# Kernel optimization log

Measured on AMD Instinct MI355X. Metric: run time of the kernel, lower is better.

Reference implementation:

```python
import jax, jax.numpy as jnp
import numpy as np

B, S, E, H = 4096, 200, 64, 128
V_U0, V_U1, V_I = 100000, 1000, 1000000

def setup_inputs() -> dict:
    key = jax.random.key(0)
    ks = jax.random.split(key, 16)
    s = 0.05
    return {
        'user_features': jax.random.randint(ks[0], (B, 2), 0, V_U1, dtype=jnp.int32),
        'target_item_features': jax.random.randint(ks[1], (B, 1), 0, V_I, dtype=jnp.int32),
        'behavior_sequence': jax.random.randint(ks[2], (B, S, 1), 0, V_I, dtype=jnp.int32),
        'emb_user0': jax.random.normal(ks[3], (V_U0, E), jnp.float32) * s,
        'emb_user1': jax.random.normal(ks[4], (V_U1, E), jnp.float32) * s,
        'emb_item': jax.random.normal(ks[5], (V_I, E), jnp.float32) * s,
        'att_w1': jax.random.normal(ks[6], (4 * E, H), jnp.float32) * s,
        'att_b1': jnp.zeros((H,), jnp.float32),
        'att_w2': jax.random.normal(ks[7], (H, 1), jnp.float32) * s,
        'att_b2': jnp.zeros((1,), jnp.float32),
        'fc_w1': jax.random.normal(ks[8], (4 * E, H), jnp.float32) * s,
        'fc_b1': jnp.zeros((H,), jnp.float32),
        'fc_w2': jax.random.normal(ks[9], (H, 1), jnp.float32) * s,
        'fc_b2': jnp.zeros((1,), jnp.float32),
    }

def reference(user_features, target_item_features, behavior_sequence,
              emb_user0, emb_user1, emb_item,
              att_w1, att_b1, att_w2, att_b2,
              fc_w1, fc_b1, fc_w2, fc_b2):
    # embedding gathers
    user_embeds = jnp.concatenate([emb_user0[user_features[:, 0]],
                                   emb_user1[user_features[:, 1]]], axis=-1)  # [B, 2E]
    target = emb_item[target_item_features[:, 0]]                              # [B, E]
    behavior = emb_item[behavior_sequence[:, :, 0]]                            # [B, S, E]
    t = target[:, None, :]                                                     # [B, 1, E]
    t_exp = jnp.broadcast_to(t, behavior.shape)
    att_in = jnp.concatenate([behavior, t_exp, behavior - t, behavior * t], axis=-1)  # [B, S, 4E]
    # attention MLP -> scores
    h = jax.nn.relu(jnp.einsum('bsd,dh->bsh', att_in, att_w1) + att_b1)
    scores = (jnp.einsum('bsh,ho->bso', h, att_w2) + att_b2)[..., 0]           # [B, S]
    weights = jax.nn.softmax(scores, axis=1)
    user_interest = jnp.einsum('bse,bs->be', behavior, weights)                # [B, E]
    combined = jnp.concatenate([user_embeds, user_interest, target], axis=-1)  # [B, 4E]
    out = jax.nn.relu(combined @ fc_w1 + fc_b1) @ fc_w2 + fc_b2                # [B, 1]
    return out
```

## Files before the change

kernel.cpp:

```cpp
#include <hip/hip_runtime.h>
#include <math.h>


#define S_LEN 200
#define S_PAD 208

typedef __attribute__((ext_vector_type(8))) short short8;
typedef __attribute__((ext_vector_type(4))) float f32x4;

__device__ __forceinline__ unsigned short f2b(float f) {
  union { float f; unsigned u; } x; x.f = f;
  unsigned r = x.u + 0x7fffu + ((x.u >> 16) & 1u);
  return (unsigned short)(r >> 16);
}
__device__ __forceinline__ float b2f(unsigned short h) {
  union { unsigned u; float f; } x; x.u = ((unsigned)h) << 16; return x.f;
}
__device__ __forceinline__ unsigned cvt_pk_bf16(float lo, float hi) {
  unsigned r;
  asm("v_cvt_pk_bf16_f32 %0, %1, %2" : "=v"(r) : "v"(lo), "v"(hi));
  return r;
}

__device__ __forceinline__ int swzB(int row, int col) {
  int byte = row * 128 + col * 2;
  byte ^= (row & 7) << 4;
  return byte >> 1;
}
__device__ __forceinline__ int swzW(int row, int col) {
  int byte = row * 512 + col * 2;
  byte ^= (row & 7) << 4;
  return byte >> 1;
}

__device__ __forceinline__ void async_g2l_16(const void* g, void* l) {
  __builtin_amdgcn_global_load_lds(
      (const __attribute__((address_space(1))) void*)g,
      (__attribute__((address_space(3))) void*)l, 16, 0, 0);
}

template <int CTRL>
__device__ __forceinline__ float dpp_add(float v) {
  const int t = __builtin_amdgcn_mov_dpp(__float_as_int(v), CTRL, 0xF, 0xF, true);
  return v + __int_as_float(t);
}
__device__ __forceinline__ float rowReduce16(float v) {
  v = dpp_add<0xB1>(v);
  v = dpp_add<0x4E>(v);
  v = dpp_add<0x124>(v);
  v = dpp_add<0x128>(v);
  return v;
}
__device__ __forceinline__ float permAdd16(float p) {
  float a = p, b = p;
  asm("v_permlane16_swap_b32 %0, %1" : "+v"(a), "+v"(b));
  return a + b;
}
__device__ __forceinline__ float permAdd32(float p) {
  float a = p, b = p;
  asm("v_permlane32_swap_b32 %0, %1" : "+v"(a), "+v"(b));
  return a + b;
}
__device__ __forceinline__ float waveSum64(float v) {
  return permAdd32(permAdd16(rowReduce16(v)));
}

#define WS_COMB 0
#define WS_AT   2097152
#define WS_DT   2113536
#define WS_BM   2129920
#define WS_FW1T 2146304
#define WS_CH   2211840
#define WS_TS   4308992

__global__ __launch_bounds__(256)
void din_prep(const float* __restrict__ aw1, const float* __restrict__ fw1,
              char* __restrict__ ws)
{
  unsigned short* ATc  = (unsigned short*)(ws + WS_AT);
  unsigned short* DTc  = (unsigned short*)(ws + WS_DT);
  unsigned short* Bm   = (unsigned short*)(ws + WS_BM);
  unsigned short* FW1T = (unsigned short*)(ws + WS_FW1T);
  const int blk = blockIdx.x, tid = threadIdx.x;

  if (blk < 32) {
    const int i = blk * 256 + tid;
    const int h = i >> 6, d = i & 63;
    const float a  = aw1[d * 128 + h];
    const float c  = aw1[(128 + d) * 128 + h];
    const float dd = aw1[(192 + d) * 128 + h];
    const int hg = h >> 5, ht = (h >> 4) & 1, hl = h & 15;
    const int kk = d >> 5, rq = (d >> 3) & 3, j = d & 7;
    const int o = (hg * 2 + ht) * 1024 + kk * 512 + rq * 128 + hl * 8 + j;
    ATc[o] = f2b(a + c);
    DTc[o] = f2b(dd);
  } else if (blk < 64) {
    const int jj = (blk - 32) * 256 + tid;
    const int d = jj >> 7, h = jj & 127;
    Bm[jj] = f2b(aw1[(64 + d) * 128 + h] - aw1[(128 + d) * 128 + h]);
  } else {
    const int i = (blk - 64) * 256 + tid;
    const int o = 2 * i;
    const int h = o >> 9;
    const int rr = o & 511;
    const int d = (rr ^ ((h & 7) << 4)) >> 1;
    FW1T[i] = f2b(fw1[d * 128 + h]);
  }
}

__global__ __launch_bounds__(128)
void din_prep2(const int* __restrict__ uf, const int* __restrict__ tif,
               const float* __restrict__ e0, const float* __restrict__ e1,
               const float* __restrict__ ei, const float* __restrict__ ab1,
               char* __restrict__ ws)
{
  __shared__ float sTt[64];
  const unsigned short* Bm = (const unsigned short*)(ws + WS_BM);
  unsigned short* combS = (unsigned short*)(ws + WS_COMB);
  float* CHW = (float*)(ws + WS_CH);
  float* TS  = (float*)(ws + WS_TS);

  const int b = blockIdx.x, tid = threadIdx.x;
  const int ti = tif[b];

  if (tid < 64) {
    const float tv = ei[(size_t)ti * 64 + tid];
    sTt[tid] = tv;
    TS[(size_t)b * 64 + tid] = tv;
    const int u0 = uf[2 * b], u1 = uf[2 * b + 1];
    unsigned short* ct = combS + (size_t)(b >> 4) * 4096;
    const int row = b & 15;
    ct[swzW(row, 192 + tid)] = f2b(tv);
    ct[swzW(row, tid)]       = f2b(e0[(size_t)u0 * 64 + tid]);
    ct[swzW(row, 64 + tid)]  = f2b(e1[(size_t)u1 * 64 + tid]);
  }
  __syncthreads();

  const int h = tid;
  float c = ab1[h];
#pragma unroll 8
  for (int d = 0; d < 64; ++d)
    c = fmaf(sTt[d], b2f(Bm[d * 128 + h]), c);
  CHW[(size_t)b * 128 + h] = c;
}

__global__ __launch_bounds__(256, 4)
void din_main(const int* __restrict__ bseq, const float* __restrict__ ei,
              const float* __restrict__ aw2, char* __restrict__ ws)
{
  __shared__ unsigned short sBeh[13312];
  __shared__ float sPart[4][S_PAD];
  __shared__ float sScores[S_PAD];
  __shared__ float sPool[4][64];
  __shared__ float sRedS[4];

  unsigned short* combS = (unsigned short*)(ws + WS_COMB);
  const unsigned short* ATc = (const unsigned short*)(ws + WS_AT);
  const unsigned short* DTc = (const unsigned short*)(ws + WS_DT);
  const float* CHW = (const float*)(ws + WS_CH);
  const float* TS  = (const float*)(ws + WS_TS);

  const int b    = blockIdx.x;
  const int tid  = threadIdx.x;
  const int lane = tid & 63;
  const int wv   = tid >> 6;
  const int hl   = lane & 15;
  const int rq   = lane >> 4;

  float4 gv[13];
#pragma unroll
  for (int it = 0; it < 13; ++it) {
    const int row = it * 16 + (tid >> 4);
    if (row < S_LEN) {
      const int idx = bseq[b * S_LEN + row];
      gv[it] = *(const float4*)(ei + (size_t)idx * 64 + (tid & 15) * 4);
    }
  }
  __builtin_amdgcn_sched_barrier(0);

  if (tid < 128) {
    const int row = 200 + (tid >> 4), c = (tid & 15) * 4;
    ushort4 z = {0, 0, 0, 0};
    *(ushort4*)&sBeh[swzB(row, c)] = z;
  }

  const float4 w2v0 = *(const float4*)(aw2 + wv * 32 + rq * 4);
  const float4 w2v1 = *(const float4*)(aw2 + wv * 32 + 16 + rq * 4);
  const f32x4 cH40 = *(const f32x4*)(CHW + (size_t)b * 128 + wv * 32 + rq * 4);
  const f32x4 cH41 = *(const f32x4*)(CHW + (size_t)b * 128 + wv * 32 + 16 + rq * 4);

  short8 w[2][2];
#pragma unroll
  for (int kk = 0; kk < 2; ++kk) {
    const float* tb = TS + (size_t)b * 64 + kk * 32 + rq * 8;
    const float4 x = *(const float4*)tb;
    const float4 y = *(const float4*)(tb + 4);
    const float tt[8] = {x.x, x.y, x.z, x.w, y.x, y.y, y.z, y.w};
#pragma unroll
    for (int ht = 0; ht < 2; ++ht) {
      const int fo = (wv * 2 + ht) * 1024 + kk * 512 + lane * 8;
      const short8 a8 = *(const short8*)(ATc + fo);
      const short8 d8 = *(const short8*)(DTc + fo);
      union { short8 s; unsigned u[4]; } o;
#pragma unroll
      for (int p = 0; p < 4; ++p) {
        const float lo = fmaf(tt[2*p],   b2f((unsigned short)d8[2*p]),   b2f((unsigned short)a8[2*p]));
        const float hi = fmaf(tt[2*p+1], b2f((unsigned short)d8[2*p+1]), b2f((unsigned short)a8[2*p+1]));
        o.u[p] = cvt_pk_bf16(lo, hi);
      }
      w[ht][kk] = o.s;
    }
  }

#pragma unroll
  for (int it = 0; it < 13; ++it) {
    const int row = it * 16 + (tid >> 4);
    if (row < S_LEN) {
      const float4 v = gv[it];
      uint2 pk;
      pk.x = cvt_pk_bf16(v.x, v.y);
      pk.y = cvt_pk_bf16(v.z, v.w);
      *(uint2*)&sBeh[swzB(row, (tid & 15) * 4)] = pk;
    }
  }
  __syncthreads();

#pragma unroll 2
  for (int tile = 0; tile < 13; ++tile) {
    const short8 av0 = *(const short8*)&sBeh[swzB(tile * 16 + hl, rq * 8)];
    const short8 av1 = *(const short8*)&sBeh[swzB(tile * 16 + hl, 32 + rq * 8)];
    f32x4 acc = cH40;
    acc = __builtin_amdgcn_mfma_f32_16x16x32_bf16(w[0][0], av0, acc, 0, 0, 0);
    acc = __builtin_amdgcn_mfma_f32_16x16x32_bf16(w[0][1], av1, acc, 0, 0, 0);
    float p;
    p = fmaxf(acc[0], 0.f) * w2v0.x;
    p = fmaf(fmaxf(acc[1], 0.f), w2v0.y, p);
    p = fmaf(fmaxf(acc[2], 0.f), w2v0.z, p);
    p = fmaf(fmaxf(acc[3], 0.f), w2v0.w, p);
    f32x4 acc2 = cH41;
    acc2 = __builtin_amdgcn_mfma_f32_16x16x32_bf16(w[1][0], av0, acc2, 0, 0, 0);
    acc2 = __builtin_amdgcn_mfma_f32_16x16x32_bf16(w[1][1], av1, acc2, 0, 0, 0);
    p = fmaf(fmaxf(acc2[0], 0.f), w2v1.x, p);
    p = fmaf(fmaxf(acc2[1], 0.f), w2v1.y, p);
    p = fmaf(fmaxf(acc2[2], 0.f), w2v1.z, p);
    p = fmaf(fmaxf(acc2[3], 0.f), w2v1.w, p);
    p = permAdd32(permAdd16(p));
    if (lane < 16) sPart[wv][tile * 16 + lane] = p;
  }
  __syncthreads();

  float e = 0.f;
  if (tid < S_PAD) {
    if (tid < S_LEN)
      e = __expf((sPart[0][tid] + sPart[1][tid]) + (sPart[2][tid] + sPart[3][tid]));
    sScores[tid] = e;
  }
  {
    const float s = waveSum64(e);
    if (lane == 0) sRedS[wv] = s;
  }
  __syncthreads();

  const float invS = 1.f / (sRedS[0] + sRedS[1] + sRedS[2] + sRedS[3]);

  {
    const int e2 = lane & 31, rr = lane >> 5;
    float p0 = 0.f, p1 = 0.f;
#pragma unroll
    for (int k = 0; k < 13; ++k) {
      const int base = 16 * k + 4 * wv + 2 * rr;
      const float2 sc2 = *(const float2*)&sScores[base];
      const unsigned u0 = *(const unsigned*)&sBeh[swzB(base, e2 * 2)];
      p0 = fmaf(sc2.x, __int_as_float((int)(u0 << 16)), p0);
      p1 = fmaf(sc2.x, __int_as_float((int)(u0 & 0xffff0000u)), p1);
      const unsigned u1 = *(const unsigned*)&sBeh[swzB(base + 1, e2 * 2)];
      p0 = fmaf(sc2.y, __int_as_float((int)(u1 << 16)), p0);
      p1 = fmaf(sc2.y, __int_as_float((int)(u1 & 0xffff0000u)), p1);
    }
    p0 = permAdd32(p0);
    p1 = permAdd32(p1);
    if (lane < 32) {
      float2 pr; pr.x = p0; pr.y = p1;
      *(float2*)&sPool[wv][e2 * 2] = pr;
    }
  }
  __syncthreads();

  if (tid < 64) {
    const float a = sPool[0][tid] + sPool[1][tid] + sPool[2][tid] + sPool[3][tid];
    combS[(size_t)(b >> 4) * 4096 + swzW(b & 15, 128 + tid)] = f2b(a * invS);
  }
}

__global__ __launch_bounds__(256, 2)
void din_fc(const float* __restrict__ fb1, const float* __restrict__ fw2,
            const float* __restrict__ fb2, const char* __restrict__ ws,
            float* __restrict__ out)
{
  __shared__ unsigned short sW[32768];
  __shared__ unsigned short sA[4096];
  __shared__ float sO[64];

  const int tid  = threadIdx.x;
  const int lane = tid & 63;
  const int wv   = tid >> 6;
  const int bb   = blockIdx.x * 16;

  {
    const char* srcW = ws + WS_FW1T;
    char* dstW = (char*)sW;
#pragma unroll
    for (int it = 0; it < 16; ++it)
      async_g2l_16(srcW + it * 4096 + tid * 16, dstW + it * 4096 + tid * 16);
    const char* srcA = ws + WS_COMB + (size_t)blockIdx.x * 8192;
    char* dstA = (char*)sA;
    async_g2l_16(srcA + tid * 16, dstA + tid * 16);
    async_g2l_16(srcA + 4096 + tid * 16, dstA + 4096 + tid * 16);
  }
  __syncthreads();

  const int hl = lane & 15, rq = lane >> 4;
  const int h0 = wv * 32 + hl, h1 = h0 + 16;
  f32x4 acc0 = {0.f, 0.f, 0.f, 0.f};
  f32x4 acc1 = {0.f, 0.f, 0.f, 0.f};
#pragma unroll
  for (int kk = 0; kk < 8; ++kk) {
    const short8 av = *(const short8*)&sA[swzW(hl, kk * 32 + rq * 8)];
    const short8 b0 = *(const short8*)&sW[swzW(h0, kk * 32 + rq * 8)];
    const short8 b1 = *(const short8*)&sW[swzW(h1, kk * 32 + rq * 8)];
    acc0 = __builtin_amdgcn_mfma_f32_16x16x32_bf16(av, b0, acc0, 0, 0, 0);
    acc1 = __builtin_amdgcn_mfma_f32_16x16x32_bf16(av, b1, acc1, 0, 0, 0);
  }
  const float fb10 = fb1[h0], fb11 = fb1[h1];
  const float fw20 = fw2[h0], fw21 = fw2[h1];
#pragma unroll
  for (int r = 0; r < 4; ++r) {
    float v = fmaxf(acc0[r] + fb10, 0.f) * fw20
            + fmaxf(acc1[r] + fb11, 0.f) * fw21;
    v += __shfl_xor(v, 1, 64);
    v += __shfl_xor(v, 2, 64);
    v += __shfl_xor(v, 4, 64);
    v += __shfl_xor(v, 8, 64);
    if (hl == 0) sO[wv * 16 + rq * 4 + r] = v;
  }
  __syncthreads();
  if (tid < 16)
    out[bb + tid] = sO[tid] + sO[16 + tid] + sO[32 + tid] + sO[48 + tid] + fb2[0];
}

extern "C" void kernel_launch(void* const* d_in, const int* in_sizes, int n_in,
                              void* d_out, int out_size, void* d_ws, size_t ws_size,
                              hipStream_t stream) {
  const int*   uf   = (const int*)d_in[0];
  const int*   tif  = (const int*)d_in[1];
  const int*   bseq = (const int*)d_in[2];
  const float* e0   = (const float*)d_in[3];
  const float* e1   = (const float*)d_in[4];
  const float* ei   = (const float*)d_in[5];
  const float* aw1  = (const float*)d_in[6];
  const float* ab1  = (const float*)d_in[7];
  const float* aw2  = (const float*)d_in[8];
  const float* fw1  = (const float*)d_in[10];
  const float* fb1  = (const float*)d_in[11];
  const float* fw2  = (const float*)d_in[12];
  const float* fb2  = (const float*)d_in[13];
  float* o = (float*)d_out;
  char* ws = (char*)d_ws;

  din_prep<<<dim3(192), dim3(256), 0, stream>>>(aw1, fw1, ws);
  din_prep2<<<dim3(4096), dim3(128), 0, stream>>>(uf, tif, e0, e1, ei, ab1, ws);
  din_main<<<dim3(4096), dim3(256), 0, stream>>>(bseq, ei, aw2, ws);
  din_fc<<<dim3(256), dim3(256), 0, stream>>>(fb1, fw2, fb2, ws, o);
}
```

Baseline: 63.48 us.

## Fuse per-batch target prep into main kernel and compute bias term with MFMA

```diff
diff --git a/kernel.cpp b/kernel.cpp
--- a/kernel.cpp
+++ b/kernel.cpp
@@ -70,8 +70,6 @@
 #define WS_DT   2113536
 #define WS_BM   2129920
 #define WS_FW1T 2146304
-#define WS_CH   2211840
-#define WS_TS   4308992
 
 __global__ __launch_bounds__(256)
 void din_prep(const float* __restrict__ aw1, const float* __restrict__ fw1,
@@ -79,25 +77,25 @@
 {
   unsigned short* ATc  = (unsigned short*)(ws + WS_AT);
   unsigned short* DTc  = (unsigned short*)(ws + WS_DT);
-  unsigned short* Bm   = (unsigned short*)(ws + WS_BM);
+  unsigned short* BMc  = (unsigned short*)(ws + WS_BM);
   unsigned short* FW1T = (unsigned short*)(ws + WS_FW1T);
   const int blk = blockIdx.x, tid = threadIdx.x;
 
-  if (blk < 32) {
-    const int i = blk * 256 + tid;
+  if (blk < 64) {
+    const int i = (blk & 31) * 256 + tid;
     const int h = i >> 6, d = i & 63;
-    const float a  = aw1[d * 128 + h];
-    const float c  = aw1[(128 + d) * 128 + h];
-    const float dd = aw1[(192 + d) * 128 + h];
     const int hg = h >> 5, ht = (h >> 4) & 1, hl = h & 15;
     const int kk = d >> 5, rq = (d >> 3) & 3, j = d & 7;
     const int o = (hg * 2 + ht) * 1024 + kk * 512 + rq * 128 + hl * 8 + j;
-    ATc[o] = f2b(a + c);
-    DTc[o] = f2b(dd);
-  } else if (blk < 64) {
-    const int jj = (blk - 32) * 256 + tid;
-    const int d = jj >> 7, h = jj & 127;
-    Bm[jj] = f2b(aw1[(64 + d) * 128 + h] - aw1[(128 + d) * 128 + h]);
+    if (blk < 32) {
+      const float a  = aw1[d * 128 + h];
+      const float c  = aw1[(128 + d) * 128 + h];
+      const float dd = aw1[(192 + d) * 128 + h];
+      ATc[o] = f2b(a + c);
+      DTc[o] = f2b(dd);
+    } else {
+      BMc[o] = f2b(aw1[(64 + d) * 128 + h] - aw1[(128 + d) * 128 + h]);
+    }
   } else {
     const int i = (blk - 64) * 256 + tid;
     const int o = 2 * i;
@@ -108,45 +106,13 @@
   }
 }
 
-__global__ __launch_bounds__(128)
-void din_prep2(const int* __restrict__ uf, const int* __restrict__ tif,
-               const float* __restrict__ e0, const float* __restrict__ e1,
-               const float* __restrict__ ei, const float* __restrict__ ab1,
-               char* __restrict__ ws)
-{
-  __shared__ float sTt[64];
-  const unsigned short* Bm = (const unsigned short*)(ws + WS_BM);
-  unsigned short* combS = (unsigned short*)(ws + WS_COMB);
-  float* CHW = (float*)(ws + WS_CH);
-  float* TS  = (float*)(ws + WS_TS);
-
-  const int b = blockIdx.x, tid = threadIdx.x;
-  const int ti = tif[b];
-
-  if (tid < 64) {
-    const float tv = ei[(size_t)ti * 64 + tid];
-    sTt[tid] = tv;
-    TS[(size_t)b * 64 + tid] = tv;
-    const int u0 = uf[2 * b], u1 = uf[2 * b + 1];
-    unsigned short* ct = combS + (size_t)(b >> 4) * 4096;
-    const int row = b & 15;
-    ct[swzW(row, 192 + tid)] = f2b(tv);
-    ct[swzW(row, tid)]       = f2b(e0[(size_t)u0 * 64 + tid]);
-    ct[swzW(row, 64 + tid)]  = f2b(e1[(size_t)u1 * 64 + tid]);
-  }
-  __syncthreads();
-
-  const int h = tid;
-  float c = ab1[h];
-#pragma unroll 8
-  for (int d = 0; d < 64; ++d)
-    c = fmaf(sTt[d], b2f(Bm[d * 128 + h]), c);
-  CHW[(size_t)b * 128 + h] = c;
-}
-
 __global__ __launch_bounds__(256, 4)
-void din_main(const int* __restrict__ bseq, const float* __restrict__ ei,
-              const float* __restrict__ aw2, char* __restrict__ ws)
+void din_main(const int* __restrict__ uf, const int* __restrict__ tif,
+              const int* __restrict__ bseq,
+              const float* __restrict__ e0, const float* __restrict__ e1,
+              const float* __restrict__ ei,
+              const float* __restrict__ ab1, const float* __restrict__ aw2,
+              char* __restrict__ ws)
 {
   __shared__ unsigned short sBeh[13312];
   __shared__ float sPart[4][S_PAD];
@@ -157,8 +123,7 @@
   unsigned short* combS = (unsigned short*)(ws + WS_COMB);
   const unsigned short* ATc = (const unsigned short*)(ws + WS_AT);
   const unsigned short* DTc = (const unsigned short*)(ws + WS_DT);
-  const float* CHW = (const float*)(ws + WS_CH);
-  const float* TS  = (const float*)(ws + WS_TS);
+  const unsigned short* BMc = (const unsigned short*)(ws + WS_BM);
 
   const int b    = blockIdx.x;
   const int tid  = threadIdx.x;
@@ -167,6 +132,8 @@
   const int hl   = lane & 15;
   const int rq   = lane >> 4;
 
+  const int ti = tif[b];
+
   float4 gv[13];
 #pragma unroll
   for (int it = 0; it < 13; ++it) {
@@ -176,6 +143,11 @@
       gv[it] = *(const float4*)(ei + (size_t)idx * 64 + (tid & 15) * 4);
     }
   }
+  const float* trow = ei + (size_t)ti * 64;
+  const float4 tx0 = *(const float4*)(trow + rq * 8);
+  const float4 tx1 = *(const float4*)(trow + rq * 8 + 4);
+  const float4 ty0 = *(const float4*)(trow + 32 + rq * 8);
+  const float4 ty1 = *(const float4*)(trow + 32 + rq * 8 + 4);
   __builtin_amdgcn_sched_barrier(0);
 
   if (tid < 128) {
@@ -184,32 +156,55 @@
     *(ushort4*)&sBeh[swzB(row, c)] = z;
   }
 
+  {
+    unsigned short* ct = combS + (size_t)(b >> 4) * 4096;
+    const int row = b & 15;
+    if (tid < 64) {
+      const int u0 = uf[2 * b];
+      ct[swzW(row, tid)] = f2b(e0[(size_t)u0 * 64 + tid]);
+    } else if (tid < 128) {
+      const int u1 = uf[2 * b + 1];
+      ct[swzW(row, 64 + (tid - 64))] = f2b(e1[(size_t)u1 * 64 + (tid - 64)]);
+    } else if (tid < 192) {
+      ct[swzW(row, 192 + (tid - 128))] = f2b(trow[tid - 128]);
+    }
+  }
+
   const float4 w2v0 = *(const float4*)(aw2 + wv * 32 + rq * 4);
   const float4 w2v1 = *(const float4*)(aw2 + wv * 32 + 16 + rq * 4);
-  const f32x4 cH40 = *(const f32x4*)(CHW + (size_t)b * 128 + wv * 32 + rq * 4);
-  const f32x4 cH41 = *(const f32x4*)(CHW + (size_t)b * 128 + wv * 32 + 16 + rq * 4);
-
+  const f32x4 abv0 = *(const f32x4*)(ab1 + wv * 32 + rq * 4);
+  const f32x4 abv1 = *(const f32x4*)(ab1 + wv * 32 + 16 + rq * 4);
+
+  const float tt0[8] = {tx0.x, tx0.y, tx0.z, tx0.w, tx1.x, tx1.y, tx1.z, tx1.w};
+  const float tt1[8] = {ty0.x, ty0.y, ty0.z, ty0.w, ty1.x, ty1.y, ty1.z, ty1.w};
   short8 w[2][2];
 #pragma unroll
-  for (int kk = 0; kk < 2; ++kk) {
-    const float* tb = TS + (size_t)b * 64 + kk * 32 + rq * 8;
-    const float4 x = *(const float4*)tb;
-    const float4 y = *(const float4*)(tb + 4);
-    const float tt[8] = {x.x, x.y, x.z, x.w, y.x, y.y, y.z, y.w};
-#pragma unroll
-    for (int ht = 0; ht < 2; ++ht) {
+  for (int ht = 0; ht < 2; ++ht) {
+#pragma unroll
+    for (int kk = 0; kk < 2; ++kk) {
       const int fo = (wv * 2 + ht) * 1024 + kk * 512 + lane * 8;
       const short8 a8 = *(const short8*)(ATc + fo);
       const short8 d8 = *(const short8*)(DTc + fo);
+      const float* tk = kk ? tt1 : tt0;
       union { short8 s; unsigned u[4]; } o;
 #pragma unroll
       for (int p = 0; p < 4; ++p) {
-        const float lo = fmaf(tt[2*p],   b2f((unsigned short)d8[2*p]),   b2f((unsigned short)a8[2*p]));
-        const float hi = fmaf(tt[2*p+1], b2f((unsigned short)d8[2*p+1]), b2f((unsigned short)a8[2*p+1]));
+        const float lo = fmaf(tk[2*p],   b2f((unsigned short)d8[2*p]),   b2f((unsigned short)a8[2*p]));
+        const float hi = fmaf(tk[2*p+1], b2f((unsigned short)d8[2*p+1]), b2f((unsigned short)a8[2*p+1]));
         o.u[p] = cvt_pk_bf16(lo, hi);
       }
       w[ht][kk] = o.s;
     }
+  }
+  short8 ttB0, ttB1;
+  {
+    union { short8 s; unsigned u[4]; } o;
+#pragma unroll
+    for (int p = 0; p < 4; ++p) o.u[p] = cvt_pk_bf16(tt0[2*p], tt0[2*p+1]);
+    ttB0 = o.s;
+#pragma unroll
+    for (int p = 0; p < 4; ++p) o.u[p] = cvt_pk_bf16(tt1[2*p], tt1[2*p+1]);
+    ttB1 = o.s;
   }
 
 #pragma unroll
@@ -223,13 +218,32 @@
       *(uint2*)&sBeh[swzB(row, (tid & 15) * 4)] = pk;
     }
   }
+
+  f32x4 accInit0, accInit1;
+  {
+    const f32x4 z = {0.f, 0.f, 0.f, 0.f};
+    f32x4 c0 = z, c1 = z;
+    const short8 bm00 = *(const short8*)(BMc + (wv * 2) * 1024 + lane * 8);
+    const short8 bm01 = *(const short8*)(BMc + (wv * 2) * 1024 + 512 + lane * 8);
+    const short8 bm10 = *(const short8*)(BMc + (wv * 2 + 1) * 1024 + lane * 8);
+    const short8 bm11 = *(const short8*)(BMc + (wv * 2 + 1) * 1024 + 512 + lane * 8);
+    c0 = __builtin_amdgcn_mfma_f32_16x16x32_bf16(bm00, ttB0, c0, 0, 0, 0);
+    c0 = __builtin_amdgcn_mfma_f32_16x16x32_bf16(bm01, ttB1, c0, 0, 0, 0);
+    c1 = __builtin_amdgcn_mfma_f32_16x16x32_bf16(bm10, ttB0, c1, 0, 0, 0);
+    c1 = __builtin_amdgcn_mfma_f32_16x16x32_bf16(bm11, ttB1, c1, 0, 0, 0);
+#pragma unroll
+    for (int r = 0; r < 4; ++r) {
+      accInit0[r] = c0[r] + abv0[r];
+      accInit1[r] = c1[r] + abv1[r];
+    }
+  }
   __syncthreads();
 
 #pragma unroll 2
   for (int tile = 0; tile < 13; ++tile) {
     const short8 av0 = *(const short8*)&sBeh[swzB(tile * 16 + hl, rq * 8)];
     const short8 av1 = *(const short8*)&sBeh[swzB(tile * 16 + hl, 32 + rq * 8)];
-    f32x4 acc = cH40;
+    f32x4 acc = accInit0;
     acc = __builtin_amdgcn_mfma_f32_16x16x32_bf16(w[0][0], av0, acc, 0, 0, 0);
     acc = __builtin_amdgcn_mfma_f32_16x16x32_bf16(w[0][1], av1, acc, 0, 0, 0);
     float p;
@@ -237,7 +251,7 @@
     p = fmaf(fmaxf(acc[1], 0.f), w2v0.y, p);
     p = fmaf(fmaxf(acc[2], 0.f), w2v0.z, p);
     p = fmaf(fmaxf(acc[3], 0.f), w2v0.w, p);
-    f32x4 acc2 = cH41;
+    f32x4 acc2 = accInit1;
     acc2 = __builtin_amdgcn_mfma_f32_16x16x32_bf16(w[1][0], av0, acc2, 0, 0, 0);
     acc2 = __builtin_amdgcn_mfma_f32_16x16x32_bf16(w[1][1], av1, acc2, 0, 0, 0);
     p = fmaf(fmaxf(acc2[0], 0.f), w2v1.x, p);
@@ -368,7 +382,7 @@
   char* ws = (char*)d_ws;
 
   din_prep<<<dim3(192), dim3(256), 0, stream>>>(aw1, fw1, ws);
-  din_prep2<<<dim3(4096), dim3(128), 0, stream>>>(uf, tif, e0, e1, ei, ab1, ws);
-  din_main<<<dim3(4096), dim3(256), 0, stream>>>(bseq, ei, aw2, ws);
+  din_main<<<dim3(4096), dim3(256), 0, stream>>>(uf, tif, bseq, e0, e1, ei,
+                                                 ab1, aw2, ws);
   din_fc<<<dim3(256), dim3(256), 0, stream>>>(fb1, fw2, fb2, ws, o);
 }
```

After: 62.74 us, median of 2. Within noise of the previous version (-1.2%).
